# Performance work log

Measured on AMD Instinct MI355X. Metric: run time of the kernel, lower is better.

The kernel has to match this reference:

```python
import jax, jax.numpy as jnp
import numpy as np

N_RES = 300000
N_RESTYPE = 21
MAX_RIGID = 8
MAX_ATOM = 24


def setup_inputs() -> dict:
    key = jax.random.key(0)
    ks = jax.random.split(key, 6)
    bb = jax.random.normal(ks[0], (N_RES, 7), dtype=jnp.float32)
    sc = jax.random.normal(ks[1], (N_RES, MAX_RIGID - 1, 2), dtype=jnp.float32)
    pos0 = jax.random.normal(ks[2], (N_RES, 3), dtype=jnp.float32)
    transforms_tensor = jax.random.normal(ks[3], (N_RESTYPE, MAX_RIGID, 4, 3), dtype=jnp.float32)
    rigids_tensor = jax.random.normal(ks[4], (N_RESTYPE, MAX_ATOM, 3), dtype=jnp.float32)
    residue_type = jax.random.randint(ks[5], (N_RES,), 0, N_RESTYPE, dtype=jnp.int32)
    # dependency tables: each rigid group depends on an earlier group (valid tree)
    rng = np.random.default_rng(0)
    td = np.zeros((N_RESTYPE, MAX_RIGID), dtype=np.int32)
    for i in range(1, MAX_RIGID):
        td[:, i] = rng.integers(0, i, size=N_RESTYPE)
    rd = rng.integers(0, MAX_RIGID, size=(N_RESTYPE, MAX_ATOM)).astype(np.int32)
    return {
        "bb": bb, "sc": sc, "pos0": pos0,
        "transforms_tensor": transforms_tensor, "rigids_tensor": rigids_tensor,
        "residue_type": residue_type,
        "transforms_dep": jnp.asarray(td), "rigids_dep": jnp.asarray(rd),
    }


def _quat_to_rot(q):
    # q: [N,4] (w,x,y,z) -> R: [N,3,3], same formulas as the torch code
    w, x, y, z = q[:, 0], q[:, 1], q[:, 2], q[:, 3]
    r00 = w * w + x * x - y * y - z * z
    r11 = w * w - x * x + y * y - z * z
    r22 = w * w - x * x - y * y + z * z
    r01 = 2 * (x * y - w * z)
    r02 = 2 * (x * z + w * y)
    r10 = 2 * (x * y + w * z)
    r12 = 2 * (y * z - w * x)
    r20 = 2 * (x * z - w * y)
    r21 = 2 * (y * z + w * x)
    return jnp.stack([
        jnp.stack([r00, r01, r02], -1),
        jnp.stack([r10, r11, r12], -1),
        jnp.stack([r20, r21, r22], -1),
    ], axis=-2)


def _combine(X, Y):
    # X, Y: [..., 4, 3] affine ops: rows 0:3 = rotation, row 3 = translation
    Rn = jnp.einsum("...ij,...jk->...ik", X[..., :3, :], Y[..., :3, :])
    tn = jnp.einsum("...ij,...j->...i", X[..., :3, :], Y[..., 3, :]) + X[..., 3, :]
    return jnp.concatenate([Rn, tn[..., None, :]], axis=-2)


def reference(bb, sc, pos0, transforms_tensor, rigids_tensor,
              residue_type, transforms_dep, rigids_dep):
    # gather per-residue constants (irregular access)
    transforms = transforms_tensor[residue_type]   # [N, MAX_RIGID, 4, 3]
    tdep = transforms_dep[residue_type]            # [N, MAX_RIGID]
    rigids = rigids_tensor[residue_type]           # [N, MAX_ATOM, 3]
    rdep = rigids_dep[residue_type]                # [N, MAX_ATOM]

    # backbone frame: quaternion -> rotation, translation 0.1*t + pos0
    R0 = _quat_to_rot(bb[:, :4])                   # [N,3,3]
    t0 = 0.1 * bb[:, 4:] + pos0                    # [N,3]
    opr0 = jnp.concatenate([R0, t0[:, None, :]], axis=1)  # [N,4,3]

    # torsion frames: rotation about x-axis by (cos,sin)=sc, zero translation
    c, s = sc[..., 0], sc[..., 1]                  # [N, MAX_RIGID-1]
    zr, on = jnp.zeros_like(c), jnp.ones_like(c)
    row0 = jnp.stack([on, zr, zr], -1)
    row1 = jnp.stack([zr, c, -s], -1)
    row2 = jnp.stack([zr, s, c], -1)
    row3 = jnp.stack([zr, zr, zr], -1)
    sc_opr = jnp.stack([row0, row1, row2, row3], axis=2)  # [N, MAX_RIGID-1, 4, 3]

    opr = jnp.concatenate([opr0[:, None], sc_opr], axis=1)  # [N, MAX_RIGID, 4, 3]
    opr = _combine(transforms, opr)

    # recursive kinematic-chain composition along the data-dependent tree
    for i_tor in range(1, MAX_RIGID):
        prev = jnp.take_along_axis(opr, tdep[:, i_tor][:, None, None, None], axis=1)[:, 0]
        opr = opr.at[:, i_tor].set(_combine(prev, opr[:, i_tor]))

    # gather each atom's frame and place atom coordinates
    opr_g = jnp.take_along_axis(opr, rdep[:, :, None, None], axis=1)  # [N, MAX_ATOM, 4, 3]
    R = jnp.einsum("naij,naj->nai", opr_g[:, :, :3, :], rigids) + opr_g[:, :, 3, :]
    return R, opr[:, 0]
```

## Files before the change

kernel.cpp:

```cpp
#include <hip/hip_runtime.h>

#define N_RES     300000
#define N_RESTYPE 21

#define TFM_STRIDE  100
#define RIG_STRIDE  76
#define TDEP_STRIDE 9
#define RDEP_STRIDE 25

typedef float f4u __attribute__((ext_vector_type(4), aligned(4)));
typedef float f2u __attribute__((ext_vector_type(2), aligned(4)));

__device__ __forceinline__ void ld12(const float* p, float* X) {
    const float4* q = reinterpret_cast<const float4*>(p);
    float4 a = q[0], b = q[1], c = q[2];
    X[0]=a.x; X[1]=a.y; X[2]=a.z;  X[3]=a.w;
    X[4]=b.x; X[5]=b.y; X[6]=b.z;  X[7]=b.w;
    X[8]=c.x; X[9]=c.y; X[10]=c.z; X[11]=c.w;
}

__device__ __forceinline__ void combine_full(const float* X, const float* Y, float* D) {
    float R[9], t[3];
    #pragma unroll
    for (int r = 0; r < 3; ++r) {
        #pragma unroll
        for (int c = 0; c < 3; ++c) {
            R[r*3+c] = X[r*3+0]*Y[0+c] + X[r*3+1]*Y[3+c] + X[r*3+2]*Y[6+c];
        }
        t[r] = X[r*3+0]*Y[9] + X[r*3+1]*Y[10] + X[r*3+2]*Y[11] + X[9+r];
    }
    #pragma unroll
    for (int k = 0; k < 9; ++k) D[k] = R[k];
    D[9]=t[0]; D[10]=t[1]; D[11]=t[2];
}

__global__ __launch_bounds__(256, 2) void backbone_kernel(
    const float* __restrict__ bb,
    const float* __restrict__ sc,
    const float* __restrict__ pos0,
    const float* __restrict__ tfm,
    const float* __restrict__ rig,
    const int*   __restrict__ rtype,
    const int*   __restrict__ tdep,
    const int*   __restrict__ rdep,
    float*       __restrict__ out)
{
    __shared__ __align__(16) float lds_tfm [N_RESTYPE * TFM_STRIDE];
    __shared__ __align__(16) float lds_rig [N_RESTYPE * RIG_STRIDE];
    __shared__ int   lds_tdep[N_RESTYPE * TDEP_STRIDE];
    __shared__ int   lds_rdep[N_RESTYPE * RDEP_STRIDE];

    const int tid = threadIdx.x;
    for (int idx = tid; idx < N_RESTYPE * 96; idx += 256) {
        int r = idx / 96; int c = idx - r * 96;
        lds_tfm[r * TFM_STRIDE + c] = tfm[idx];
    }
    for (int idx = tid; idx < N_RESTYPE * 72; idx += 256) {
        int r = idx / 72; int c = idx - r * 72;
        lds_rig[r * RIG_STRIDE + c] = rig[idx];
    }
    for (int idx = tid; idx < N_RESTYPE * 8; idx += 256) {
        int r = idx >> 3; int c = idx & 7;
        lds_tdep[r * TDEP_STRIDE + c] = tdep[idx];
    }
    for (int idx = tid; idx < N_RESTYPE * 24; idx += 256) {
        int r = idx / 24; int c = idx - r * 24;
        lds_rdep[r * RDEP_STRIDE + c] = rdep[idx];
    }
    __syncthreads();

    const int n = blockIdx.x * 256 + tid;
    if (n >= N_RES) return;

    const int rt = rtype[n];

    const float* bbn = bb + (size_t)n * 7;
    f4u bv0 = *reinterpret_cast<const f4u*>(bbn);
    f4u bv1 = *reinterpret_cast<const f4u*>(bbn + 3);
    float w = bv0.x, x = bv0.y, y = bv0.z, z = bv0.w;

    const float* pn = pos0 + (size_t)n * 3;
    f2u pv = *reinterpret_cast<const f2u*>(pn);
    float t0x = 0.1f * bv1.y + pv.x;
    float t0y = 0.1f * bv1.z + pv.y;
    float t0z = 0.1f * bv1.w + pn[2];

    const float* scn = sc + (size_t)n * 14;
    f4u s0 = *reinterpret_cast<const f4u*>(scn);
    f4u s1 = *reinterpret_cast<const f4u*>(scn + 4);
    f4u s2 = *reinterpret_cast<const f4u*>(scn + 8);
    f2u s3 = *reinterpret_cast<const f2u*>(scn + 12);
    float csc[7] = {s0.x, s0.z, s1.x, s1.z, s2.x, s2.z, s3.x};
    float css[7] = {s0.y, s0.w, s1.y, s1.w, s2.y, s2.w, s3.y};

    float ww = w*w, xx = x*x, yy = y*y, zz = z*z;
    float xy = x*y, wz = w*z, xz = x*z, wy = w*y, yz = y*z, wx = w*x;
    float Y0[12];
    Y0[0] = ww + xx - yy - zz;
    Y0[1] = 2.0f * (xy - wz);
    Y0[2] = 2.0f * (xz + wy);
    Y0[3] = 2.0f * (xy + wz);
    Y0[4] = ww - xx + yy - zz;
    Y0[5] = 2.0f * (yz - wx);
    Y0[6] = 2.0f * (xz - wy);
    Y0[7] = 2.0f * (yz + wx);
    Y0[8] = ww - xx - yy + zz;
    Y0[9] = t0x; Y0[10] = t0y; Y0[11] = t0z;

    float opr[8][12];
    {
        float X[12];
        ld12(&lds_tfm[rt * TFM_STRIDE], X);
        combine_full(X, Y0, opr[0]);
    }
    #pragma unroll
    for (int i = 1; i < 8; ++i) {
        float X[12];
        ld12(&lds_tfm[rt * TFM_STRIDE + i * 12], X);
        float cj = csc[i-1], sj = css[i-1];
        #pragma unroll
        for (int r = 0; r < 3; ++r) {
            opr[i][r*3+0] = X[r*3+0];
            opr[i][r*3+1] = X[r*3+1]*cj + X[r*3+2]*sj;
            opr[i][r*3+2] = X[r*3+2]*cj - X[r*3+1]*sj;
        }
        opr[i][9]  = X[9];
        opr[i][10] = X[10];
        opr[i][11] = X[11];
    }

    #pragma unroll
    for (int i = 1; i < 8; ++i) {
        int dep = lds_tdep[rt * TDEP_STRIDE + i];
        float P[12];
        #pragma unroll
        for (int k = 0; k < 12; ++k) P[k] = opr[0][k];
        #pragma unroll
        for (int j = 1; j < 8; ++j) {
            if (j < i) {
                bool m = (dep == j);
                #pragma unroll
                for (int k = 0; k < 12; ++k) P[k] = m ? opr[j][k] : P[k];
            }
        }
        combine_full(P, opr[i], opr[i]);
    }

    float ob[72];
    const float* rbase = &lds_rig[rt * RIG_STRIDE];
    #pragma unroll
    for (int g4 = 0; g4 < 6; ++g4) {
        float V[12];
        ld12(rbase + g4 * 12, V);
        #pragma unroll
        for (int aa = 0; aa < 4; ++aa) {
            int a = g4 * 4 + aa;
            int r = lds_rdep[rt * RDEP_STRIDE + a];
            bool b0 = (r & 1), b1 = (r & 2), b2 = (r & 4);
            float g[12];
            #pragma unroll
            for (int k = 0; k < 12; ++k) {
                float s01 = b0 ? opr[1][k] : opr[0][k];
                float s23 = b0 ? opr[3][k] : opr[2][k];
                float s45 = b0 ? opr[5][k] : opr[4][k];
                float s67 = b0 ? opr[7][k] : opr[6][k];
                float s0123 = b1 ? s23 : s01;
                float s4567 = b1 ? s67 : s45;
                g[k] = b2 ? s4567 : s0123;
            }
            float vx = V[aa*3+0], vy = V[aa*3+1], vz = V[aa*3+2];
            ob[a*3+0] = g[0]*vx + g[1]*vy + g[2]*vz + g[9];
            ob[a*3+1] = g[3]*vx + g[4]*vy + g[5]*vz + g[10];
            ob[a*3+2] = g[6]*vx + g[7]*vy + g[8]*vz + g[11];
        }
    }

    float4* opR = reinterpret_cast<float4*>(out + (size_t)n * 72);
    #pragma unroll
    for (int q = 0; q < 18; ++q) {
        opR[q] = make_float4(ob[q*4+0], ob[q*4+1], ob[q*4+2], ob[q*4+3]);
    }
    float4* o2 = reinterpret_cast<float4*>(out + (size_t)N_RES * 72 + (size_t)n * 12);
    o2[0] = make_float4(opr[0][0], opr[0][1], opr[0][2],  opr[0][3]);
    o2[1] = make_float4(opr[0][4], opr[0][5], opr[0][6],  opr[0][7]);
    o2[2] = make_float4(opr[0][8], opr[0][9], opr[0][10], opr[0][11]);
}

extern "C" void kernel_launch(void* const* d_in, const int* in_sizes, int n_in,
                              void* d_out, int out_size, void* d_ws, size_t ws_size,
                              hipStream_t stream) {
    const float* bb    = (const float*)d_in[0];
    const float* sc    = (const float*)d_in[1];
    const float* pos0  = (const float*)d_in[2];
    const float* tfm   = (const float*)d_in[3];
    const float* rig   = (const float*)d_in[4];
    const int*   rtype = (const int*)d_in[5];
    const int*   tdep  = (const int*)d_in[6];
    const int*   rdep  = (const int*)d_in[7];
    float* out = (float*)d_out;

    const int blocks = (N_RES + 255) / 256;
    backbone_kernel<<<blocks, 256, 0, stream>>>(bb, sc, pos0, tfm, rig,
                                                rtype, tdep, rdep, out);
}
```

Measured before the change: 165.7 us.

## Stage per-thread rigid frames in LDS instead of register select chains

Each thread's eight composed frames now live in its own slice of LDS rather than in a 96-float register array. Dependency lookups become indexed LDS loads instead of unrolled select chains across all frames. Output rows are written in chunks as each group finishes, so the 72-float output buffer no longer stays in registers. Block size drops to 128 with a higher occupancy hint. This cuts VGPR pressure and select ALU work, but adds LDS traffic, possible bank conflicts from the stride-100 per-thread layout, and a larger LDS footprint per block that may itself limit occupancy.

```diff
diff --git a/kernel.cpp b/kernel.cpp
--- a/kernel.cpp
+++ b/kernel.cpp
@@ -2,7 +2,9 @@
 
 #define N_RES     300000
 #define N_RESTYPE 21
+#define BLK       128
 
+#define OPR_STRIDE  100
 #define TFM_STRIDE  100
 #define RIG_STRIDE  76
 #define TDEP_STRIDE 9
@@ -17,6 +19,13 @@
     X[0]=a.x; X[1]=a.y; X[2]=a.z;  X[3]=a.w;
     X[4]=b.x; X[5]=b.y; X[6]=b.z;  X[7]=b.w;
     X[8]=c.x; X[9]=c.y; X[10]=c.z; X[11]=c.w;
+}
+
+__device__ __forceinline__ void st12(float* p, const float* X) {
+    float4* q = reinterpret_cast<float4*>(p);
+    q[0] = make_float4(X[0], X[1], X[2],  X[3]);
+    q[1] = make_float4(X[4], X[5], X[6],  X[7]);
+    q[2] = make_float4(X[8], X[9], X[10], X[11]);
 }
 
 __device__ __forceinline__ void combine_full(const float* X, const float* Y, float* D) {
@@ -34,7 +43,7 @@
     D[9]=t[0]; D[10]=t[1]; D[11]=t[2];
 }
 
-__global__ __launch_bounds__(256, 2) void backbone_kernel(
+__global__ __launch_bounds__(BLK, 4) void backbone_kernel(
     const float* __restrict__ bb,
     const float* __restrict__ sc,
     const float* __restrict__ pos0,
@@ -45,34 +54,36 @@
     const int*   __restrict__ rdep,
     float*       __restrict__ out)
 {
+    __shared__ __align__(16) float lds_opr [BLK * OPR_STRIDE];
     __shared__ __align__(16) float lds_tfm [N_RESTYPE * TFM_STRIDE];
     __shared__ __align__(16) float lds_rig [N_RESTYPE * RIG_STRIDE];
     __shared__ int   lds_tdep[N_RESTYPE * TDEP_STRIDE];
     __shared__ int   lds_rdep[N_RESTYPE * RDEP_STRIDE];
 
     const int tid = threadIdx.x;
-    for (int idx = tid; idx < N_RESTYPE * 96; idx += 256) {
+    for (int idx = tid; idx < N_RESTYPE * 96; idx += BLK) {
         int r = idx / 96; int c = idx - r * 96;
         lds_tfm[r * TFM_STRIDE + c] = tfm[idx];
     }
-    for (int idx = tid; idx < N_RESTYPE * 72; idx += 256) {
+    for (int idx = tid; idx < N_RESTYPE * 72; idx += BLK) {
         int r = idx / 72; int c = idx - r * 72;
         lds_rig[r * RIG_STRIDE + c] = rig[idx];
     }
-    for (int idx = tid; idx < N_RESTYPE * 8; idx += 256) {
+    for (int idx = tid; idx < N_RESTYPE * 8; idx += BLK) {
         int r = idx >> 3; int c = idx & 7;
         lds_tdep[r * TDEP_STRIDE + c] = tdep[idx];
     }
-    for (int idx = tid; idx < N_RESTYPE * 24; idx += 256) {
+    for (int idx = tid; idx < N_RESTYPE * 24; idx += BLK) {
         int r = idx / 24; int c = idx - r * 24;
         lds_rdep[r * RDEP_STRIDE + c] = rdep[idx];
     }
     __syncthreads();
 
-    const int n = blockIdx.x * 256 + tid;
+    const int n = blockIdx.x * BLK + tid;
     if (n >= N_RES) return;
 
     const int rt = rtype[n];
+    float* const myopr = &lds_opr[tid * OPR_STRIDE];
 
     const float* bbn = bb + (size_t)n * 7;
     f4u bv0 = *reinterpret_cast<const f4u*>(bbn);
@@ -107,83 +118,62 @@
     Y0[8] = ww - xx - yy + zz;
     Y0[9] = t0x; Y0[10] = t0y; Y0[11] = t0z;
 
-    float opr[8][12];
+    float opr0[12];
     {
         float X[12];
         ld12(&lds_tfm[rt * TFM_STRIDE], X);
-        combine_full(X, Y0, opr[0]);
+        combine_full(X, Y0, opr0);
+        st12(myopr, opr0);
     }
+
     #pragma unroll
     for (int i = 1; i < 8; ++i) {
-        float X[12];
+        float X[12], cur[12];
         ld12(&lds_tfm[rt * TFM_STRIDE + i * 12], X);
         float cj = csc[i-1], sj = css[i-1];
         #pragma unroll
         for (int r = 0; r < 3; ++r) {
-            opr[i][r*3+0] = X[r*3+0];
-            opr[i][r*3+1] = X[r*3+1]*cj + X[r*3+2]*sj;
-            opr[i][r*3+2] = X[r*3+2]*cj - X[r*3+1]*sj;
+            cur[r*3+0] = X[r*3+0];
+            cur[r*3+1] = X[r*3+1]*cj + X[r*3+2]*sj;
+            cur[r*3+2] = X[r*3+2]*cj - X[r*3+1]*sj;
         }
-        opr[i][9]  = X[9];
-        opr[i][10] = X[10];
-        opr[i][11] = X[11];
+        cur[9] = X[9]; cur[10] = X[10]; cur[11] = X[11];
+
+        int dep = lds_tdep[rt * TDEP_STRIDE + i];
+        float P[12];
+        ld12(myopr + dep * 12, P);
+        combine_full(P, cur, cur);
+        st12(myopr + i * 12, cur);
     }
 
-    #pragma unroll
-    for (int i = 1; i < 8; ++i) {
-        int dep = lds_tdep[rt * TDEP_STRIDE + i];
-        float P[12];
-        #pragma unroll
-        for (int k = 0; k < 12; ++k) P[k] = opr[0][k];
-        #pragma unroll
-        for (int j = 1; j < 8; ++j) {
-            if (j < i) {
-                bool m = (dep == j);
-                #pragma unroll
-                for (int k = 0; k < 12; ++k) P[k] = m ? opr[j][k] : P[k];
-            }
-        }
-        combine_full(P, opr[i], opr[i]);
-    }
-
-    float ob[72];
     const float* rbase = &lds_rig[rt * RIG_STRIDE];
+    float* outR = out + (size_t)n * 72;
     #pragma unroll
     for (int g4 = 0; g4 < 6; ++g4) {
         float V[12];
         ld12(rbase + g4 * 12, V);
+        float ob[12];
         #pragma unroll
         for (int aa = 0; aa < 4; ++aa) {
             int a = g4 * 4 + aa;
             int r = lds_rdep[rt * RDEP_STRIDE + a];
-            bool b0 = (r & 1), b1 = (r & 2), b2 = (r & 4);
             float g[12];
-            #pragma unroll
-            for (int k = 0; k < 12; ++k) {
-                float s01 = b0 ? opr[1][k] : opr[0][k];
-                float s23 = b0 ? opr[3][k] : opr[2][k];
-                float s45 = b0 ? opr[5][k] : opr[4][k];
-                float s67 = b0 ? opr[7][k] : opr[6][k];
-                float s0123 = b1 ? s23 : s01;
-                float s4567 = b1 ? s67 : s45;
-                g[k] = b2 ? s4567 : s0123;
-            }
+            ld12(myopr + r * 12, g);
             float vx = V[aa*3+0], vy = V[aa*3+1], vz = V[aa*3+2];
-            ob[a*3+0] = g[0]*vx + g[1]*vy + g[2]*vz + g[9];
-            ob[a*3+1] = g[3]*vx + g[4]*vy + g[5]*vz + g[10];
-            ob[a*3+2] = g[6]*vx + g[7]*vy + g[8]*vz + g[11];
+            ob[aa*3+0] = g[0]*vx + g[1]*vy + g[2]*vz + g[9];
+            ob[aa*3+1] = g[3]*vx + g[4]*vy + g[5]*vz + g[10];
+            ob[aa*3+2] = g[6]*vx + g[7]*vy + g[8]*vz + g[11];
         }
+        float4* op = reinterpret_cast<float4*>(outR + g4 * 12);
+        op[0] = make_float4(ob[0], ob[1], ob[2],  ob[3]);
+        op[1] = make_float4(ob[4], ob[5], ob[6],  ob[7]);
+        op[2] = make_float4(ob[8], ob[9], ob[10], ob[11]);
     }
 
-    float4* opR = reinterpret_cast<float4*>(out + (size_t)n * 72);
-    #pragma unroll
-    for (int q = 0; q < 18; ++q) {
-        opR[q] = make_float4(ob[q*4+0], ob[q*4+1], ob[q*4+2], ob[q*4+3]);
-    }
     float4* o2 = reinterpret_cast<float4*>(out + (size_t)N_RES * 72 + (size_t)n * 12);
-    o2[0] = make_float4(opr[0][0], opr[0][1], opr[0][2],  opr[0][3]);
-    o2[1] = make_float4(opr[0][4], opr[0][5], opr[0][6],  opr[0][7]);
-    o2[2] = make_float4(opr[0][8], opr[0][9], opr[0][10], opr[0][11]);
+    o2[0] = make_float4(opr0[0], opr0[1], opr0[2],  opr0[3]);
+    o2[1] = make_float4(opr0[4], opr0[5], opr0[6],  opr0[7]);
+    o2[2] = make_float4(opr0[8], opr0[9], opr0[10], opr0[11]);
 }
 
 extern "C" void kernel_launch(void* const* d_in, const int* in_sizes, int n_in,
@@ -199,7 +189,7 @@
     const int*   rdep  = (const int*)d_in[7];
     float* out = (float*)d_out;
 
-    const int blocks = (N_RES + 255) / 256;
-    backbone_kernel<<<blocks, 256, 0, stream>>>(bb, sc, pos0, tfm, rig,
+    const int blocks = (N_RES + BLK - 1) / BLK;
+    backbone_kernel<<<blocks, BLK, 0, stream>>>(bb, sc, pos0, tfm, rig,
                                                 rtype, tdep, rdep, out);
 }
```

Measured after the change: 186.3 us. +12.4%, slower.

## Drop LDS staging of lookup tables, read from global, use 64-thread blocks

Applied to the files above, without the earlier changes.

Removes the per-block shared-memory copy of the per-residue-type tables and the barrier, and reads transforms, rigids and dependency tables straight from global memory, where they should stay cache-resident. Block size drops from 256 to 64 and the launch bound changes accordingly. Atom outputs are now written per group of four atoms instead of being buffered in a 72-float array, which should cut register pressure. In exchange, each table access becomes a divergent per-thread global or scalar-cache load instead of an LDS read.

```diff
diff --git a/kernel.cpp b/kernel.cpp
--- a/kernel.cpp
+++ b/kernel.cpp
@@ -2,16 +2,12 @@
 
 #define N_RES     300000
 #define N_RESTYPE 21
-
-#define TFM_STRIDE  100
-#define RIG_STRIDE  76
-#define TDEP_STRIDE 9
-#define RDEP_STRIDE 25
+#define BLK       64
 
 typedef float f4u __attribute__((ext_vector_type(4), aligned(4)));
 typedef float f2u __attribute__((ext_vector_type(2), aligned(4)));
 
-__device__ __forceinline__ void ld12(const float* p, float* X) {
+__device__ __forceinline__ void ld12g(const float* p, float* X) {
     const float4* q = reinterpret_cast<const float4*>(p);
     float4 a = q[0], b = q[1], c = q[2];
     X[0]=a.x; X[1]=a.y; X[2]=a.z;  X[3]=a.w;
@@ -34,7 +30,7 @@
     D[9]=t[0]; D[10]=t[1]; D[11]=t[2];
 }
 
-__global__ __launch_bounds__(256, 2) void backbone_kernel(
+__global__ __launch_bounds__(BLK, 4) void backbone_kernel(
     const float* __restrict__ bb,
     const float* __restrict__ sc,
     const float* __restrict__ pos0,
@@ -45,34 +41,12 @@
     const int*   __restrict__ rdep,
     float*       __restrict__ out)
 {
-    __shared__ __align__(16) float lds_tfm [N_RESTYPE * TFM_STRIDE];
-    __shared__ __align__(16) float lds_rig [N_RESTYPE * RIG_STRIDE];
-    __shared__ int   lds_tdep[N_RESTYPE * TDEP_STRIDE];
-    __shared__ int   lds_rdep[N_RESTYPE * RDEP_STRIDE];
-
-    const int tid = threadIdx.x;
-    for (int idx = tid; idx < N_RESTYPE * 96; idx += 256) {
-        int r = idx / 96; int c = idx - r * 96;
-        lds_tfm[r * TFM_STRIDE + c] = tfm[idx];
-    }
-    for (int idx = tid; idx < N_RESTYPE * 72; idx += 256) {
-        int r = idx / 72; int c = idx - r * 72;
-        lds_rig[r * RIG_STRIDE + c] = rig[idx];
-    }
-    for (int idx = tid; idx < N_RESTYPE * 8; idx += 256) {
-        int r = idx >> 3; int c = idx & 7;
-        lds_tdep[r * TDEP_STRIDE + c] = tdep[idx];
-    }
-    for (int idx = tid; idx < N_RESTYPE * 24; idx += 256) {
-        int r = idx / 24; int c = idx - r * 24;
-        lds_rdep[r * RDEP_STRIDE + c] = rdep[idx];
-    }
-    __syncthreads();
-
-    const int n = blockIdx.x * 256 + tid;
+    const int n = blockIdx.x * BLK + threadIdx.x;
     if (n >= N_RES) return;
 
     const int rt = rtype[n];
+    const float* tbase = tfm + rt * 96;
+    const float* rbase = rig + rt * 72;
 
     const float* bbn = bb + (size_t)n * 7;
     f4u bv0 = *reinterpret_cast<const f4u*>(bbn);
@@ -110,13 +84,13 @@
     float opr[8][12];
     {
         float X[12];
-        ld12(&lds_tfm[rt * TFM_STRIDE], X);
+        ld12g(tbase, X);
         combine_full(X, Y0, opr[0]);
     }
     #pragma unroll
     for (int i = 1; i < 8; ++i) {
         float X[12];
-        ld12(&lds_tfm[rt * TFM_STRIDE + i * 12], X);
+        ld12g(tbase + i * 12, X);
         float cj = csc[i-1], sj = css[i-1];
         #pragma unroll
         for (int r = 0; r < 3; ++r) {
@@ -129,9 +103,10 @@
         opr[i][11] = X[11];
     }
 
+    const int* tdn = tdep + rt * 8;
     #pragma unroll
     for (int i = 1; i < 8; ++i) {
-        int dep = lds_tdep[rt * TDEP_STRIDE + i];
+        int dep = tdn[i];
         float P[12];
         #pragma unroll
         for (int k = 0; k < 12; ++k) P[k] = opr[0][k];
@@ -146,16 +121,17 @@
         combine_full(P, opr[i], opr[i]);
     }
 
-    float ob[72];
-    const float* rbase = &lds_rig[rt * RIG_STRIDE];
+    const int* rdn = rdep + rt * 24;
+    float* outR = out + (size_t)n * 72;
     #pragma unroll
     for (int g4 = 0; g4 < 6; ++g4) {
         float V[12];
-        ld12(rbase + g4 * 12, V);
+        ld12g(rbase + g4 * 12, V);
+        float ob[12];
         #pragma unroll
         for (int aa = 0; aa < 4; ++aa) {
             int a = g4 * 4 + aa;
-            int r = lds_rdep[rt * RDEP_STRIDE + a];
+            int r = rdn[a];
             bool b0 = (r & 1), b1 = (r & 2), b2 = (r & 4);
             float g[12];
             #pragma unroll
@@ -169,17 +145,16 @@
                 g[k] = b2 ? s4567 : s0123;
             }
             float vx = V[aa*3+0], vy = V[aa*3+1], vz = V[aa*3+2];
-            ob[a*3+0] = g[0]*vx + g[1]*vy + g[2]*vz + g[9];
-            ob[a*3+1] = g[3]*vx + g[4]*vy + g[5]*vz + g[10];
-            ob[a*3+2] = g[6]*vx + g[7]*vy + g[8]*vz + g[11];
+            ob[aa*3+0] = g[0]*vx + g[1]*vy + g[2]*vz + g[9];
+            ob[aa*3+1] = g[3]*vx + g[4]*vy + g[5]*vz + g[10];
+            ob[aa*3+2] = g[6]*vx + g[7]*vy + g[8]*vz + g[11];
         }
+        float4* op = reinterpret_cast<float4*>(outR + g4 * 12);
+        op[0] = make_float4(ob[0], ob[1], ob[2],  ob[3]);
+        op[1] = make_float4(ob[4], ob[5], ob[6],  ob[7]);
+        op[2] = make_float4(ob[8], ob[9], ob[10], ob[11]);
     }
 
-    float4* opR = reinterpret_cast<float4*>(out + (size_t)n * 72);
-    #pragma unroll
-    for (int q = 0; q < 18; ++q) {
-        opR[q] = make_float4(ob[q*4+0], ob[q*4+1], ob[q*4+2], ob[q*4+3]);
-    }
     float4* o2 = reinterpret_cast<float4*>(out + (size_t)N_RES * 72 + (size_t)n * 12);
     o2[0] = make_float4(opr[0][0], opr[0][1], opr[0][2],  opr[0][3]);
     o2[1] = make_float4(opr[0][4], opr[0][5], opr[0][6],  opr[0][7]);
@@ -199,7 +174,7 @@
     const int*   rdep  = (const int*)d_in[7];
     float* out = (float*)d_out;
 
-    const int blocks = (N_RES + 255) / 256;
-    backbone_kernel<<<blocks, 256, 0, stream>>>(bb, sc, pos0, tfm, rig,
+    const int blocks = (N_RES + BLK - 1) / BLK;
+    backbone_kernel<<<blocks, BLK, 0, stream>>>(bb, sc, pos0, tfm, rig,
                                                 rtype, tdep, rdep, out);
 }
```

Result: slower. 305.0 us (+84.1%).
